# Kernel tuning notes

Hardware: AMD Instinct MI355X
Metric: run time of the kernel (lower is better)

Reference implementation:

```python
import jax, jax.numpy as jnp
import numpy as np

B, D, H, DH = 2048, 1024, 8, 64  # batch, query_dim, heads, dim_head
INNER = H * DH  # 512


def setup_inputs() -> dict:
    key = jax.random.key(0)
    k0, k1, k2, k3 = jax.random.split(key, 4)
    x = jax.random.normal(k0, (B, D), dtype=jnp.float32)
    Wq = jax.random.normal(k1, (D, INNER), dtype=jnp.float32) * 0.02
    Wkv = jax.random.normal(k2, (D, 2 * INNER), dtype=jnp.float32) * 0.02
    Wout = jax.random.normal(k3, (INNER, D), dtype=jnp.float32) * 0.02
    bout = jnp.zeros((D,), dtype=jnp.float32)
    return {"x": x, "Wq": Wq, "Wkv": Wkv, "Wout": Wout, "bout": bout}


def reference(x, Wq, Wkv, Wout, bout):
    # Faithful to the original: 2D x, attention over the flattened (B*H) axis.
    b = x.shape[0]
    scale = DH ** -0.5
    q = (x @ Wq).reshape(b * H, DH)            # (b h) d
    k, v = jnp.split(x @ Wkv, 2, axis=-1)      # each [b, inner]
    k = k.reshape(b * H, DH)
    v = v.reshape(b * H, DH)
    sim = (q @ k.T) * scale                    # [(b h), (b h)] -- 1 GB intermediate
    attn = jax.nn.softmax(sim, axis=-1)        # dropout_rate = 0 -> identity
    out = (attn @ v).reshape(b, INNER)         # b (h d)
    return out @ Wout + bout                   # project_out path
```

## Files before the change

### kernel.cpp

```cpp
#include <hip/hip_runtime.h>
#include <hip/hip_bf16.h>
#include <stdint.h>


typedef __bf16 bf16_t;
typedef __bf16 bf16x4 __attribute__((ext_vector_type(4)));
typedef __bf16 bf16x8 __attribute__((ext_vector_type(8)));
typedef float floatx4 __attribute__((ext_vector_type(4)));

__device__ __forceinline__ floatx4 mfma16(bf16x8 a, bf16x8 b, floatx4 c) {
    return __builtin_amdgcn_mfma_f32_16x16x32_bf16(a, b, c, 0, 0, 0);
}

__device__ __forceinline__ bf16x8 cvt8(float4 a, float4 b) {
    bf16x8 o;
    o[0] = (bf16_t)a.x; o[1] = (bf16_t)a.y; o[2] = (bf16_t)a.z; o[3] = (bf16_t)a.w;
    o[4] = (bf16_t)b.x; o[5] = (bf16_t)b.y; o[6] = (bf16_t)b.z; o[7] = (bf16_t)b.w;
    return o;
}

__device__ __forceinline__ void transpose_body(const float* __restrict__ in, int N,
                                               bf16_t* __restrict__ out, int ldo,
                                               int bx, int by, int tid, float (*tile)[33]) {
    int n0 = bx * 32, k0 = by * 32;
    int tx = tid & 31, ty = tid >> 5;
#pragma unroll
    for (int i = 0; i < 32; i += 8)
        tile[ty + i][tx] = in[(size_t)(k0 + ty + i) * N + (n0 + tx)];
    __syncthreads();
#pragma unroll
    for (int i = 0; i < 32; i += 8)
        out[(size_t)(n0 + ty + i) * ldo + (k0 + tx)] = (bf16_t)tile[tx][ty + i];
}

__global__ __launch_bounds__(256) void prep_all(const float* __restrict__ x,
                                                bf16_t* __restrict__ xb,
                                                const float* __restrict__ Wq,
                                                const float* __restrict__ Wkv,
                                                const float* __restrict__ Wout,
                                                bf16_t* __restrict__ WtQKV,
                                                bf16_t* __restrict__ WtOut) {
    __shared__ float tile[32][33];
    int b = blockIdx.x, tid = threadIdx.x;
    if (b < 1024) {
        int i = (b * 256 + tid) * 8;
        *(bf16x8*)(xb + i) = cvt8(*(const float4*)(x + i), *(const float4*)(x + i + 4));
    } else if (b < 1536) {
        b -= 1024;
        transpose_body(Wq, 512, WtQKV, 1024, b & 15, b >> 4, tid, tile);
    } else if (b < 2560) {
        b -= 1536;
        transpose_body(Wkv, 1024, WtQKV + 512 * 1024, 1024, b & 31, b >> 5, tid, tile);
    } else {
        b -= 2560;
        transpose_body(Wout, 1024, WtOut, 512, b & 31, b >> 5, tid, tile);
    }
}

template <int OF32, int MI>
__global__ __launch_bounds__(256) void gemm_bt(const bf16_t* __restrict__ A,
                                               const bf16_t* __restrict__ Bt,
                                               const float* __restrict__ bias,
                                               void* __restrict__ Cout,
                                               bf16_t* __restrict__ VtOut, int vt_col0,
                                               int K, int lda, int ldb, int ldc,
                                               float qscale, int qcols) {
    constexpr int MT = MI * 32;
    constexpr int PA = MT / 64;
    __shared__ bf16_t sA[MT * 64];
    __shared__ bf16_t sB[64 * 64];
    int tid = threadIdx.x;
    int wave = tid >> 6, lane = tid & 63;
    int lm = lane & 15, q = lane >> 4;
    int bm = blockIdx.x * MT, bn = blockIdx.y * 64;
    int wm = (wave >> 1) * (MT / 2), wn = (wave & 1) * 32;

    int c0 = (tid & 3) * 2, c1 = c0 + 1;
    int rA[PA], swA[PA];
    size_t srcA0[PA], srcA1[PA];
#pragma unroll
    for (int p = 0; p < PA; ++p) {
        rA[p] = p * 64 + (tid >> 2);
        swA[p] = rA[p] & 7;
        srcA0[p] = (size_t)(bm + rA[p]) * lda + ((c0 ^ swA[p]) << 3);
        srcA1[p] = (size_t)(bm + rA[p]) * lda + ((c1 ^ swA[p]) << 3);
    }
    int rB = tid >> 2, swB = rB & 7;
    size_t srcB0 = (size_t)(bn + rB) * ldb + ((c0 ^ swB) << 3);
    size_t srcB1 = (size_t)(bn + rB) * ldb + ((c1 ^ swB) << 3);

    floatx4 acc[MI][2];
#pragma unroll
    for (int i = 0; i < MI; ++i)
#pragma unroll
        for (int j = 0; j < 2; ++j) acc[i][j] = (floatx4){0.f, 0.f, 0.f, 0.f};

    bf16x8 pa0[PA], pa1[PA], pb0, pb1;
#pragma unroll
    for (int p = 0; p < PA; ++p) {
        pa0[p] = *(const bf16x8*)(A + srcA0[p]);
        pa1[p] = *(const bf16x8*)(A + srcA1[p]);
    }
    pb0 = *(const bf16x8*)(Bt + srcB0);
    pb1 = *(const bf16x8*)(Bt + srcB1);
#pragma unroll
    for (int p = 0; p < PA; ++p) {
        *(bf16x8*)&sA[p * 4096 + tid * 16] = pa0[p];
        *(bf16x8*)&sA[p * 4096 + tid * 16 + 8] = pa1[p];
    }
    *(bf16x8*)&sB[tid * 16] = pb0;
    *(bf16x8*)&sB[tid * 16 + 8] = pb1;
    __syncthreads();

    for (int k0 = 0; k0 < K; k0 += 64) {
        int kn = (k0 + 64 < K) ? k0 + 64 : 0;
#pragma unroll
        for (int p = 0; p < PA; ++p) {
            pa0[p] = *(const bf16x8*)(A + srcA0[p] + kn);
            pa1[p] = *(const bf16x8*)(A + srcA1[p] + kn);
        }
        pb0 = *(const bf16x8*)(Bt + srcB0 + kn);
        pb1 = *(const bf16x8*)(Bt + srcB1 + kn);

#pragma unroll
        for (int s = 0; s < 2; ++s) {
            int cs = s * 4 + q;
            bf16x8 af[MI], bfr[2];
#pragma unroll
            for (int i = 0; i < MI; ++i) {
                int row = wm + i * 16 + lm;
                af[i] = *(bf16x8*)&sA[row * 64 + ((cs ^ (lm & 7)) << 3)];
            }
#pragma unroll
            for (int j = 0; j < 2; ++j) {
                int row = wn + j * 16 + lm;
                bfr[j] = *(bf16x8*)&sB[row * 64 + ((cs ^ (lm & 7)) << 3)];
            }
#pragma unroll
            for (int i = 0; i < MI; ++i)
#pragma unroll
                for (int j = 0; j < 2; ++j)
                    acc[i][j] = mfma16(af[i], bfr[j], acc[i][j]);
        }

        __syncthreads();
#pragma unroll
        for (int p = 0; p < PA; ++p) {
            *(bf16x8*)&sA[p * 4096 + tid * 16] = pa0[p];
            *(bf16x8*)&sA[p * 4096 + tid * 16 + 8] = pa1[p];
        }
        *(bf16x8*)&sB[tid * 16] = pb0;
        *(bf16x8*)&sB[tid * 16 + 8] = pb1;
        __syncthreads();
    }

#pragma unroll
    for (int i = 0; i < MI; ++i)
#pragma unroll
        for (int j = 0; j < 2; ++j)
#pragma unroll
            for (int r = 0; r < 4; ++r) {
                int row = bm + wm + i * 16 + q * 4 + r;
                int col = bn + wn + j * 16 + lm;
                float v = acc[i][j][r];
                if (col < qcols) v *= qscale;
                if (bias) v += bias[col];
                if (col >= vt_col0) {
                    int cc = col - vt_col0;
                    VtOut[(size_t)(cc & 63) * 16384 + row * 8 + (cc >> 6)] = (bf16_t)v;
                } else {
                    size_t off = (size_t)row * ldc + col;
                    if (OF32) ((float*)Cout)[off] = v;
                    else      ((bf16_t*)Cout)[off] = (bf16_t)v;
                }
            }
}

__global__ __launch_bounds__(256, 2) void flash_attn(const bf16_t* __restrict__ QK,
                                                     const bf16_t* __restrict__ Vt,
                                                     bf16_t* __restrict__ O,
                                                     float* __restrict__ accP,
                                                     float* __restrict__ lP,
                                                     int kps, int nsplit) {
    __shared__ bf16_t sK[64 * 64];
    __shared__ bf16_t sVt[64 * 64];
    int tid = threadIdx.x;
    int wave = tid >> 6, lane = tid & 63;
    int lm = lane & 15, q = lane >> 4;
    int sp = blockIdx.y;
    int qrow0 = blockIdx.x * 256 + wave * 64;

    bf16x8 qf[4][2];
#pragma unroll
    for (int sub = 0; sub < 4; ++sub) {
        int qr = qrow0 + sub * 16 + lm;
        const bf16_t* qp = QK + (size_t)(qr >> 3) * 1024 + (qr & 7) * 64;
        qf[sub][0] = *(const bf16x8*)(qp + q * 8);
        qf[sub][1] = *(const bf16x8*)(qp + 32 + q * 8);
    }

    int sr = tid >> 2;
    int ch0 = (tid & 3) * 2, ch1 = ch0 + 1;
    int swz = sr & 7;
    int lsr = 32 * (sr >> 5) + 8 * ((sr >> 2) & 3) + 4 * ((sr >> 4) & 1) + (sr & 3);
    int ksrcA = (lsr >> 3) * 1024 + (lsr & 7) * 64 + 512 + ((ch0 ^ swz) << 3);
    int ksrcB = (lsr >> 3) * 1024 + (lsr & 7) * 64 + 512 + ((ch1 ^ swz) << 3);
    size_t vsrcA = (size_t)sr * 16384 + ((ch0 ^ swz) << 3);
    size_t vsrcB = (size_t)sr * 16384 + ((ch1 ^ swz) << 3);
    bf16_t* dK = &sK[tid * 16];
    bf16_t* dV = &sVt[tid * 16];

    int c0 = q ^ (lm & 7);

    floatx4 acc[4][4];
#pragma unroll
    for (int sub = 0; sub < 4; ++sub)
#pragma unroll
        for (int i = 0; i < 4; ++i) acc[sub][i] = (floatx4){0.f, 0.f, 0.f, 0.f};
    float lacc[4] = {0.f, 0.f, 0.f, 0.f};

    int kt0 = sp * kps, kend = kt0 + kps;

    bf16x8 krA, krB, vrA, vrB;
    {
        const bf16_t* kb = QK + (size_t)kt0 * 128;
        krA = *(const bf16x8*)(kb + ksrcA);
        krB = *(const bf16x8*)(kb + ksrcB);
        vrA = *(const bf16x8*)(Vt + vsrcA + kt0);
        vrB = *(const bf16x8*)(Vt + vsrcB + kt0);
    }
    *(bf16x8*)dK = krA; *(bf16x8*)(dK + 8) = krB;
    *(bf16x8*)dV = vrA; *(bf16x8*)(dV + 8) = vrB;
    __syncthreads();

    for (int kt = kt0; kt < kend; kt += 64) {
        int ktn = (kt + 64 < kend) ? kt + 64 : kt0;
        const bf16_t* kbn = QK + (size_t)ktn * 128;
        krA = *(const bf16x8*)(kbn + ksrcA);
        krB = *(const bf16x8*)(kbn + ksrcB);
        vrA = *(const bf16x8*)(Vt + vsrcA + ktn);
        vrB = *(const bf16x8*)(Vt + vsrcB + ktn);

        floatx4 s[4][4];
#pragma unroll
        for (int nb = 0; nb < 4; ++nb) {
            int row = (nb * 16 + lm) * 64;
            bf16x8 k0 = *(bf16x8*)&sK[row + (c0 << 3)];
            bf16x8 k1 = *(bf16x8*)&sK[row + ((c0 ^ 4) << 3)];
#pragma unroll
            for (int sub = 0; sub < 4; ++sub) {
                floatx4 a = (floatx4){0.f, 0.f, 0.f, 0.f};
                a = mfma16(k0, qf[sub][0], a);
                a = mfma16(k1, qf[sub][1], a);
                s[sub][nb] = a;
            }
        }

        bf16x8 pf[4][2];
#pragma unroll
        for (int sub = 0; sub < 4; ++sub) {
#pragma unroll
            for (int nb = 0; nb < 4; ++nb)
#pragma unroll
                for (int r = 0; r < 4; ++r) {
                    float pv = __builtin_amdgcn_exp2f(s[sub][nb][r]);
                    s[sub][nb][r] = pv;
                    lacc[sub] += pv;
                }
#pragma unroll
            for (int jb = 0; jb < 2; ++jb) {
                bf16x8 p;
#pragma unroll
                for (int r = 0; r < 4; ++r) {
                    p[r] = (bf16_t)s[sub][2 * jb][r];
                    p[r + 4] = (bf16_t)s[sub][2 * jb + 1][r];
                }
                pf[sub][jb] = p;
            }
        }

#pragma unroll
        for (int jb = 0; jb < 2; ++jb) {
            bf16x8 av[4];
#pragma unroll
            for (int nd = 0; nd < 4; ++nd)
                av[nd] = *(bf16x8*)&sVt[(nd * 16 + lm) * 64 + ((c0 ^ (jb << 2)) << 3)];
#pragma unroll
            for (int sub = 0; sub < 4; ++sub)
#pragma unroll
                for (int nd = 0; nd < 4; ++nd)
                    acc[sub][nd] = mfma16(av[nd], pf[sub][jb], acc[sub][nd]);
        }

        __syncthreads();
        *(bf16x8*)dK = krA; *(bf16x8*)(dK + 8) = krB;
        *(bf16x8*)dV = vrA; *(bf16x8*)(dV + 8) = vrB;
        __syncthreads();
    }

#pragma unroll
    for (int sub = 0; sub < 4; ++sub) {
        lacc[sub] += __shfl_xor(lacc[sub], 16);
        lacc[sub] += __shfl_xor(lacc[sub], 32);
    }

    if (nsplit == 1) {
#pragma unroll
        for (int sub = 0; sub < 4; ++sub) {
            float inv = 1.f / lacc[sub];
            int row = qrow0 + sub * 16 + lm;
#pragma unroll
            for (int nd = 0; nd < 4; ++nd) {
                bf16x4 o;
#pragma unroll
                for (int r = 0; r < 4; ++r) o[r] = (bf16_t)(acc[sub][nd][r] * inv);
                *(bf16x4*)&O[(size_t)row * 64 + nd * 16 + q * 4] = o;
            }
        }
    } else {
#pragma unroll
        for (int sub = 0; sub < 4; ++sub) {
            int row = qrow0 + sub * 16 + lm;
            size_t base = ((size_t)sp * 16384 + row) * 64;
#pragma unroll
            for (int nd = 0; nd < 4; ++nd) {
                float4 v = {acc[sub][nd][0], acc[sub][nd][1],
                            acc[sub][nd][2], acc[sub][nd][3]};
                *(float4*)&accP[base + nd * 16 + q * 4] = v;
            }
            if (lane < 16) lP[sp * 16384 + row] = lacc[sub];
        }
    }
}

__global__ __launch_bounds__(256) void merge_attn(const float* __restrict__ accP,
                                                  const float* __restrict__ lP,
                                                  bf16_t* __restrict__ O, int nsplit) {
    int idx = blockIdx.x * 256 + threadIdx.x;
    int row = idx >> 4, dh4 = (idx & 15) * 4;
    float4 num = {0.f, 0.f, 0.f, 0.f};
    float den = 0.f;
    for (int s = 0; s < nsplit; ++s) {
        float4 a = *(const float4*)&accP[((size_t)s * 16384 + row) * 64 + dh4];
        num.x += a.x; num.y += a.y; num.z += a.z; num.w += a.w;
        den += lP[s * 16384 + row];
    }
    float inv = 1.f / den;
    bf16x4 o;
    o[0] = (bf16_t)(num.x * inv); o[1] = (bf16_t)(num.y * inv);
    o[2] = (bf16_t)(num.z * inv); o[3] = (bf16_t)(num.w * inv);
    *(bf16x4*)&O[(size_t)row * 64 + dh4] = o;
}

extern "C" void kernel_launch(void* const* d_in, const int* in_sizes, int n_in,
                              void* d_out, int out_size, void* d_ws, size_t ws_size,
                              hipStream_t stream) {
    const float* x    = (const float*)d_in[0];
    const float* Wq   = (const float*)d_in[1];
    const float* Wkv  = (const float*)d_in[2];
    const float* Wout = (const float*)d_in[3];
    const float* bout = (const float*)d_in[4];

    char* ws = (char*)d_ws;
    bf16_t* QK    = (bf16_t*)ws;
    bf16_t* Vt    = (bf16_t*)(ws + 4194304);
    bf16_t* Ob    = (bf16_t*)(ws + 6291456);
    bf16_t* xb    = (bf16_t*)(ws + 8388608);
    bf16_t* WtQKV = (bf16_t*)(ws + 12582912);
    bf16_t* WtOut = (bf16_t*)(ws + 15728640);
    float*  accP  = (float*)(ws + 16777216);

    int nsplit = (ws_size >= (size_t)16777216 + 8 * 4259840) ? 8
               : (ws_size >= (size_t)16777216 + 4 * 4259840) ? 4
               : (ws_size >= (size_t)16777216 + 2 * 4259840) ? 2 : 1;
    float* lP = (float*)(ws + 16777216 + (size_t)nsplit * 4194304);

    prep_all<<<3072, 256, 0, stream>>>(x, xb, Wq, Wkv, Wout, WtQKV, WtOut);

    gemm_bt<0, 2><<<dim3(32, 24), 256, 0, stream>>>(
        xb, WtQKV, nullptr, QK, Vt, 1024, 1024, 1024, 1024, 1024,
        0.18033688011112042f, 512);

    flash_attn<<<dim3(64, nsplit), 256, 0, stream>>>(QK, Vt, Ob, accP, lP,
                                                     16384 / nsplit, nsplit);
    if (nsplit > 1)
        merge_attn<<<1024, 256, 0, stream>>>(accP, lP, Ob, nsplit);

    gemm_bt<1, 2><<<dim3(32, 16), 256, 0, stream>>>(
        Ob, WtOut, bout, d_out, nullptr, 1 << 30, 512, 512, 512, 1024,
        1.0f, 0);
}
```

Before: 171.3 us.

## Deepen GEMM global prefetch to two tiles and allow 16-way attention split

The GEMM main loop now keeps two register sets of prefetched tiles and unrolls by two, so global loads are issued two K-steps ahead of the compute instead of one. This is meant to hide more global memory latency, at the cost of more registers and extra barriers per step. The workspace is also repacked so attention partial accumulators reuse the region of xb and WtQKV, which are dead once the QKV GEMM has run. That lets the split-K flash attention use up to 16 splits when the workspace is large enough, adding parallelism over the key axis in exchange for more merge work.

```diff
diff --git a/kernel.cpp b/kernel.cpp
--- a/kernel.cpp
+++ b/kernel.cpp
@@ -95,33 +95,28 @@
 #pragma unroll
         for (int j = 0; j < 2; ++j) acc[i][j] = (floatx4){0.f, 0.f, 0.f, 0.f};
 
-    bf16x8 pa0[PA], pa1[PA], pb0, pb1;
-#pragma unroll
-    for (int p = 0; p < PA; ++p) {
-        pa0[p] = *(const bf16x8*)(A + srcA0[p]);
-        pa1[p] = *(const bf16x8*)(A + srcA1[p]);
-    }
-    pb0 = *(const bf16x8*)(Bt + srcB0);
-    pb1 = *(const bf16x8*)(Bt + srcB1);
-#pragma unroll
-    for (int p = 0; p < PA; ++p) {
-        *(bf16x8*)&sA[p * 4096 + tid * 16] = pa0[p];
-        *(bf16x8*)&sA[p * 4096 + tid * 16 + 8] = pa1[p];
-    }
-    *(bf16x8*)&sB[tid * 16] = pb0;
-    *(bf16x8*)&sB[tid * 16 + 8] = pb1;
-    __syncthreads();
-
-    for (int k0 = 0; k0 < K; k0 += 64) {
-        int kn = (k0 + 64 < K) ? k0 + 64 : 0;
+    bf16x8 pa0A[PA], pa1A[PA], pb0A, pb1A;
+    bf16x8 pa0B[PA], pa1B[PA], pb0B, pb1B;
+
+    auto load_set = [&](int kn, bf16x8 a0[PA], bf16x8 a1[PA], bf16x8& b0, bf16x8& b1) {
 #pragma unroll
         for (int p = 0; p < PA; ++p) {
-            pa0[p] = *(const bf16x8*)(A + srcA0[p] + kn);
-            pa1[p] = *(const bf16x8*)(A + srcA1[p] + kn);
-        }
-        pb0 = *(const bf16x8*)(Bt + srcB0 + kn);
-        pb1 = *(const bf16x8*)(Bt + srcB1 + kn);
-
+            a0[p] = *(const bf16x8*)(A + srcA0[p] + kn);
+            a1[p] = *(const bf16x8*)(A + srcA1[p] + kn);
+        }
+        b0 = *(const bf16x8*)(Bt + srcB0 + kn);
+        b1 = *(const bf16x8*)(Bt + srcB1 + kn);
+    };
+    auto deposit_set = [&](bf16x8 a0[PA], bf16x8 a1[PA], bf16x8 b0, bf16x8 b1) {
+#pragma unroll
+        for (int p = 0; p < PA; ++p) {
+            *(bf16x8*)&sA[p * 4096 + tid * 16] = a0[p];
+            *(bf16x8*)&sA[p * 4096 + tid * 16 + 8] = a1[p];
+        }
+        *(bf16x8*)&sB[tid * 16] = b0;
+        *(bf16x8*)&sB[tid * 16 + 8] = b1;
+    };
+    auto compute_tile = [&]() {
 #pragma unroll
         for (int s = 0; s < 2; ++s) {
             int cs = s * 4 + q;
@@ -142,15 +137,26 @@
                 for (int j = 0; j < 2; ++j)
                     acc[i][j] = mfma16(af[i], bfr[j], acc[i][j]);
         }
-
-        __syncthreads();
-#pragma unroll
-        for (int p = 0; p < PA; ++p) {
-            *(bf16x8*)&sA[p * 4096 + tid * 16] = pa0[p];
-            *(bf16x8*)&sA[p * 4096 + tid * 16 + 8] = pa1[p];
-        }
-        *(bf16x8*)&sB[tid * 16] = pb0;
-        *(bf16x8*)&sB[tid * 16 + 8] = pb1;
+    };
+
+    load_set(0, pa0A, pa1A, pb0A, pb1A);
+    deposit_set(pa0A, pa1A, pb0A, pb1A);
+    load_set(64 < K ? 64 : 0, pa0B, pa1B, pb0B, pb1B);
+    __syncthreads();
+
+    for (int kt = 0; kt < K; kt += 128) {
+        int k2 = (kt + 128 < K) ? kt + 128 : 0;
+        load_set(k2, pa0A, pa1A, pb0A, pb1A);
+        compute_tile();
+        __syncthreads();
+        deposit_set(pa0B, pa1B, pb0B, pb1B);
+        __syncthreads();
+
+        int k3 = (kt + 192 < K) ? kt + 192 : 0;
+        load_set(k3, pa0B, pa1B, pb0B, pb1B);
+        compute_tile();
+        __syncthreads();
+        deposit_set(pa0A, pa1A, pb0A, pb1A);
         __syncthreads();
     }
 
@@ -365,15 +371,16 @@
     bf16_t* QK    = (bf16_t*)ws;
     bf16_t* Vt    = (bf16_t*)(ws + 4194304);
     bf16_t* Ob    = (bf16_t*)(ws + 6291456);
-    bf16_t* xb    = (bf16_t*)(ws + 8388608);
-    bf16_t* WtQKV = (bf16_t*)(ws + 12582912);
-    bf16_t* WtOut = (bf16_t*)(ws + 15728640);
-    float*  accP  = (float*)(ws + 16777216);
-
-    int nsplit = (ws_size >= (size_t)16777216 + 8 * 4259840) ? 8
-               : (ws_size >= (size_t)16777216 + 4 * 4259840) ? 4
-               : (ws_size >= (size_t)16777216 + 2 * 4259840) ? 2 : 1;
-    float* lP = (float*)(ws + 16777216 + (size_t)nsplit * 4194304);
+    bf16_t* WtOut = (bf16_t*)(ws + 8388608);
+    bf16_t* xb    = (bf16_t*)(ws + 9437184);
+    bf16_t* WtQKV = (bf16_t*)(ws + 13631488);
+    float*  accP  = (float*)(ws + 9437184);
+
+    int nsplit = (ws_size >= (size_t)9437184 + 16 * 4259840) ? 16
+               : (ws_size >= (size_t)9437184 + 8 * 4259840)  ? 8
+               : (ws_size >= (size_t)9437184 + 4 * 4259840)  ? 4
+               : (ws_size >= (size_t)9437184 + 2 * 4259840)  ? 2 : 1;
+    float* lP = (float*)(ws + 9437184 + (size_t)nsplit * 4194304);
 
     prep_all<<<3072, 256, 0, stream>>>(x, xb, Wq, Wkv, Wout, WtQKV, WtOut);
 
```

New measurement: 177.8 us. 3.8% more time.

## Interleave QK/exp/PV per half-tile, raise occupancy, allow 16-way KV split

Applied to the files above, without the earlier changes.

The attention inner loop now computes scores, exponentials and the PV MFMAs one 32-key half at a time, instead of materialising all 16 score tiles first. This cuts live registers so launch bounds can be raised to 3 waves-groups per SIMD. The workspace layout is also compacted, reusing the xb/WtQKV region for split accumulators so a 16-way KV split fits. The risks are register spills under the tighter bound, and extra merge traffic from more splits.

```diff
diff --git a/kernel.cpp b/kernel.cpp
--- a/kernel.cpp
+++ b/kernel.cpp
@@ -176,7 +176,7 @@
             }
 }
 
-__global__ __launch_bounds__(256, 2) void flash_attn(const bf16_t* __restrict__ QK,
+__global__ __launch_bounds__(256, 3) void flash_attn(const bf16_t* __restrict__ QK,
                                                      const bf16_t* __restrict__ Vt,
                                                      bf16_t* __restrict__ O,
                                                      float* __restrict__ accP,
@@ -241,55 +241,42 @@
         vrA = *(const bf16x8*)(Vt + vsrcA + ktn);
         vrB = *(const bf16x8*)(Vt + vsrcB + ktn);
 
-        floatx4 s[4][4];
-#pragma unroll
-        for (int nb = 0; nb < 4; ++nb) {
-            int row = (nb * 16 + lm) * 64;
-            bf16x8 k0 = *(bf16x8*)&sK[row + (c0 << 3)];
-            bf16x8 k1 = *(bf16x8*)&sK[row + ((c0 ^ 4) << 3)];
-#pragma unroll
-            for (int sub = 0; sub < 4; ++sub) {
-                floatx4 a = (floatx4){0.f, 0.f, 0.f, 0.f};
-                a = mfma16(k0, qf[sub][0], a);
-                a = mfma16(k1, qf[sub][1], a);
-                s[sub][nb] = a;
-            }
-        }
-
-        bf16x8 pf[4][2];
-#pragma unroll
-        for (int sub = 0; sub < 4; ++sub) {
-#pragma unroll
-            for (int nb = 0; nb < 4; ++nb)
-#pragma unroll
-                for (int r = 0; r < 4; ++r) {
-                    float pv = __builtin_amdgcn_exp2f(s[sub][nb][r]);
-                    s[sub][nb][r] = pv;
-                    lacc[sub] += pv;
+#pragma unroll
+        for (int jb = 0; jb < 2; ++jb) {
+            floatx4 s[4][2];
+#pragma unroll
+            for (int p2 = 0; p2 < 2; ++p2) {
+                int nb = jb * 2 + p2;
+                int row = (nb * 16 + lm) * 64;
+                bf16x8 k0 = *(bf16x8*)&sK[row + (c0 << 3)];
+                bf16x8 k1 = *(bf16x8*)&sK[row + ((c0 ^ 4) << 3)];
+#pragma unroll
+                for (int sub = 0; sub < 4; ++sub) {
+                    floatx4 a = (floatx4){0.f, 0.f, 0.f, 0.f};
+                    a = mfma16(k0, qf[sub][0], a);
+                    a = mfma16(k1, qf[sub][1], a);
+                    s[sub][p2] = a;
                 }
-#pragma unroll
-            for (int jb = 0; jb < 2; ++jb) {
-                bf16x8 p;
-#pragma unroll
-                for (int r = 0; r < 4; ++r) {
-                    p[r] = (bf16_t)s[sub][2 * jb][r];
-                    p[r + 4] = (bf16_t)s[sub][2 * jb + 1][r];
-                }
-                pf[sub][jb] = p;
-            }
-        }
-
-#pragma unroll
-        for (int jb = 0; jb < 2; ++jb) {
+            }
             bf16x8 av[4];
 #pragma unroll
             for (int nd = 0; nd < 4; ++nd)
                 av[nd] = *(bf16x8*)&sVt[(nd * 16 + lm) * 64 + ((c0 ^ (jb << 2)) << 3)];
 #pragma unroll
-            for (int sub = 0; sub < 4; ++sub)
+            for (int sub = 0; sub < 4; ++sub) {
+                bf16x8 p;
+#pragma unroll
+                for (int r = 0; r < 4; ++r) {
+                    float p0 = __builtin_amdgcn_exp2f(s[sub][0][r]);
+                    float p1 = __builtin_amdgcn_exp2f(s[sub][1][r]);
+                    lacc[sub] += p0 + p1;
+                    p[r] = (bf16_t)p0;
+                    p[r + 4] = (bf16_t)p1;
+                }
 #pragma unroll
                 for (int nd = 0; nd < 4; ++nd)
-                    acc[sub][nd] = mfma16(av[nd], pf[sub][jb], acc[sub][nd]);
+                    acc[sub][nd] = mfma16(av[nd], p, acc[sub][nd]);
+            }
         }
 
         __syncthreads();
@@ -365,15 +352,16 @@
     bf16_t* QK    = (bf16_t*)ws;
     bf16_t* Vt    = (bf16_t*)(ws + 4194304);
     bf16_t* Ob    = (bf16_t*)(ws + 6291456);
-    bf16_t* xb    = (bf16_t*)(ws + 8388608);
-    bf16_t* WtQKV = (bf16_t*)(ws + 12582912);
-    bf16_t* WtOut = (bf16_t*)(ws + 15728640);
-    float*  accP  = (float*)(ws + 16777216);
-
-    int nsplit = (ws_size >= (size_t)16777216 + 8 * 4259840) ? 8
-               : (ws_size >= (size_t)16777216 + 4 * 4259840) ? 4
-               : (ws_size >= (size_t)16777216 + 2 * 4259840) ? 2 : 1;
-    float* lP = (float*)(ws + 16777216 + (size_t)nsplit * 4194304);
+    bf16_t* WtOut = (bf16_t*)(ws + 8388608);
+    bf16_t* xb    = (bf16_t*)(ws + 9437184);
+    bf16_t* WtQKV = (bf16_t*)(ws + 13631488);
+    float*  accP  = (float*)(ws + 9437184);
+
+    int nsplit = (ws_size >= (size_t)9437184 + 16 * 4259840) ? 16
+               : (ws_size >= (size_t)9437184 + 8 * 4259840)  ? 8
+               : (ws_size >= (size_t)9437184 + 4 * 4259840)  ? 4
+               : (ws_size >= (size_t)9437184 + 2 * 4259840)  ? 2 : 1;
+    float* lP = (float*)(ws + 9437184 + (size_t)nsplit * 4194304);
 
     prep_all<<<3072, 256, 0, stream>>>(x, xb, Wq, Wkv, Wout, WtQKV, WtOut);
 
```

After: 373.3 us. 2.18x slower.
